# Kernel tuning notes

Measured on AMD Instinct MI355X. Metric: run time of the kernel, lower is better.

## Reference

```python
import jax, jax.numpy as jnp
import numpy as np

B, S, M = 128, 4096, 20
LOG_2PI = float(np.log(2.0 * np.pi))


def setup_inputs() -> dict:
    key = jax.random.key(0)
    k1, k2, k3, k4, k5 = jax.random.split(key, 5)
    xs = jax.random.normal(k1, (B, S, 5), dtype=jnp.float32)
    logits_pred = jax.random.normal(k2, (B, S, M), dtype=jnp.float32)
    mus_pred = jax.random.normal(k3, (B, S, M, 2), dtype=jnp.float32)
    # sigmas are Cholesky entries (l00, l10, l11); diagonal must be positive.
    sigmas_pred = jax.random.uniform(k4, (B, S, M, 3), dtype=jnp.float32) + 0.1
    pen_pred = jax.random.uniform(k5, (B, S, 3), dtype=jnp.float32)
    return {"xs": xs, "logits_pred": logits_pred, "mus_pred": mus_pred,
            "sigmas_pred": sigmas_pred, "pen_pred": pen_pred}


def reference(xs, logits_pred, mus_pred, sigmas_pred, pen_pred):
    # split stroke-5 format: (dx_abs, dy_abs) + 3 pen states
    position_true = xs[..., :2]          # [B,S,2]
    pen_true = xs[..., 2:]               # [B,S,3]

    # relative positions: roll by 1 along seq, first step prev = (0,0)
    position_prev = jnp.concatenate(
        [jnp.zeros_like(position_true[:, :1]), position_true[:, :-1]], axis=1)
    rel = position_true - position_prev  # [B,S,2]

    # closed-form 2D Gaussian log-density with lower-tri Cholesky
    # scale_tril entries (tril_indices(2,2) order): l00, l10, l11
    l00 = sigmas_pred[..., 0]            # [B,S,M]
    l10 = sigmas_pred[..., 1]
    l11 = sigmas_pred[..., 2]
    d = rel[:, :, None, :] - mus_pred    # [B,S,M,2]
    z0 = d[..., 0] / l00
    z1 = (d[..., 1] - l10 * z0) / l11
    comp_logp = (-0.5 * (z0 * z0 + z1 * z1)
                 - LOG_2PI - jnp.log(l00) - jnp.log(l11))  # [B,S,M]

    # mixture log-prob via logsumexp over components
    mix_logp = jax.nn.logsumexp(
        jax.nn.log_softmax(logits_pred, axis=-1) + comp_logp, axis=-1)  # [B,S]
    position_loss = -jnp.sum(mix_logp)

    # pen loss: faithful to source -> CrossEntropyLoss(input=pen_true, target=pen_pred)
    # (soft-target CE, mean reduction over B*S rows)
    logp = jax.nn.log_softmax(pen_true.reshape(-1, 3), axis=-1)
    pen_loss = jnp.mean(-jnp.sum(pen_pred.reshape(-1, 3) * logp, axis=-1))

    return position_loss + pen_loss
```

## Files before the change

kernel.cpp:

```cpp
#include <hip/hip_runtime.h>
#include <math.h>

#define BB 128
#define SS 4096
#define MM 20
#define NPOS (BB * SS)
#define BLOCK 256
#define NBLOCKS (NPOS / BLOCK)

__device__ __forceinline__ float fast_rcp(float x) { return __builtin_amdgcn_rcpf(x); }

__global__ __launch_bounds__(BLOCK) void sketch_main(
    const float* __restrict__ xs,
    const float* __restrict__ logits,
    const float* __restrict__ mus,
    const float* __restrict__ sigmas,
    const float* __restrict__ pen_pred,
    float* __restrict__ partials)
{
    const float LOG_2PI = 1.8378770664093453f;
    int idx = blockIdx.x * BLOCK + threadIdx.x;
    int s = idx & (SS - 1);

    const float* xp = xs + (size_t)idx * 5;
    float px  = xp[0], py  = xp[1];
    float pt0 = xp[2], pt1 = xp[3], pt2 = xp[4];
    float qx = 0.0f, qy = 0.0f;
    if (s != 0) { qx = xp[-5]; qy = xp[-4]; }
    float rx = px - qx, ry = py - qy;

    const float4* lp = (const float4*)(logits + (size_t)idx * 20);
    float lg[20];
#pragma unroll
    for (int i = 0; i < 5; ++i) {
        float4 v = lp[i];
        lg[4*i+0]=v.x; lg[4*i+1]=v.y; lg[4*i+2]=v.z; lg[4*i+3]=v.w;
    }
    const float4* mp = (const float4*)(mus + (size_t)idx * 40);
    float mu[40];
#pragma unroll
    for (int i = 0; i < 10; ++i) {
        float4 v = mp[i];
        mu[4*i+0]=v.x; mu[4*i+1]=v.y; mu[4*i+2]=v.z; mu[4*i+3]=v.w;
    }
    const float4* sp = (const float4*)(sigmas + (size_t)idx * 60);
    float sg[60];
#pragma unroll
    for (int i = 0; i < 15; ++i) {
        float4 v = sp[i];
        sg[4*i+0]=v.x; sg[4*i+1]=v.y; sg[4*i+2]=v.z; sg[4*i+3]=v.w;
    }

    float a[20];
    float mx_l = -INFINITY, mx_a = -INFINITY;
#pragma unroll
    for (int m = 0; m < MM; ++m) {
        float l00 = sg[3*m+0], l10 = sg[3*m+1], l11 = sg[3*m+2];
        float dx = rx - mu[2*m+0];
        float dy = ry - mu[2*m+1];
        float z0 = dx * fast_rcp(l00);
        float z1 = (dy - l10 * z0) * fast_rcp(l11);
        float comp = -0.5f * (z0*z0 + z1*z1) - LOG_2PI - __logf(l00 * l11);
        float av = lg[m] + comp;
        a[m] = av;
        mx_l = fmaxf(mx_l, lg[m]);
        mx_a = fmaxf(mx_a, av);
    }
    float se_l = 0.0f, se_a = 0.0f;
#pragma unroll
    for (int m = 0; m < MM; ++m) {
        se_l += __expf(lg[m] - mx_l);
        se_a += __expf(a[m]  - mx_a);
    }
    float mix_logp = (mx_a + __logf(se_a)) - (mx_l + __logf(se_l));

    float pm = fmaxf(pt0, fmaxf(pt1, pt2));
    float es = __expf(pt0 - pm) + __expf(pt1 - pm) + __expf(pt2 - pm);
    float lse3 = pm + __logf(es);
    const float* pp = pen_pred + (size_t)idx * 3;
    float pen = -(pp[0]*(pt0-lse3) + pp[1]*(pt1-lse3) + pp[2]*(pt2-lse3));

    float val = -mix_logp + pen * (1.0f / (float)NPOS);

#pragma unroll
    for (int off = 32; off > 0; off >>= 1) val += __shfl_down(val, off, 64);
    __shared__ float red[BLOCK / 64];
    int lane = threadIdx.x & 63, wid = threadIdx.x >> 6;
    if (lane == 0) red[wid] = val;
    __syncthreads();
    if (threadIdx.x == 0)
        partials[blockIdx.x] = red[0] + red[1] + red[2] + red[3];
}

__global__ __launch_bounds__(BLOCK) void sketch_reduce(
    const float* __restrict__ partials, float* __restrict__ out)
{
    float v = 0.0f;
    for (int i = threadIdx.x; i < NBLOCKS; i += BLOCK) v += partials[i];
#pragma unroll
    for (int off = 32; off > 0; off >>= 1) v += __shfl_down(v, off, 64);
    __shared__ float red[BLOCK / 64];
    int lane = threadIdx.x & 63, wid = threadIdx.x >> 6;
    if (lane == 0) red[wid] = v;
    __syncthreads();
    if (threadIdx.x == 0)
        out[0] = red[0] + red[1] + red[2] + red[3];
}

extern "C" void kernel_launch(void* const* d_in, const int* in_sizes, int n_in,
                              void* d_out, int out_size, void* d_ws, size_t ws_size,
                              hipStream_t stream) {
    const float* xs       = (const float*)d_in[0];
    const float* logits   = (const float*)d_in[1];
    const float* mus      = (const float*)d_in[2];
    const float* sigmas   = (const float*)d_in[3];
    const float* pen_pred = (const float*)d_in[4];
    float* out = (float*)d_out;
    float* partials = (float*)d_ws;

    sketch_main<<<NBLOCKS, BLOCK, 0, stream>>>(xs, logits, mus, sigmas, pen_pred, partials);
    sketch_reduce<<<1, BLOCK, 0, stream>>>(partials, out);
}
```

Measured before the change: 295.9 us.

## Map mixture components to lanes with half-wave shuffle reductions

Instead of one thread handling a whole position with 120 floats in registers, each half-wave of 32 lanes now handles one position, one lane per mixture component. Max and sum reductions run through xor shuffles, and each wave loops over 64 positions. The goal is contiguous loads across lanes, lower register pressure and better occupancy. In exchange 12 of every 32 lanes sit idle, and each position pays for shuffle reductions and redundant xs/pen loads that every lane performs.

```diff
diff --git a/kernel.cpp b/kernel.cpp
--- a/kernel.cpp
+++ b/kernel.cpp
@@ -6,7 +6,9 @@
 #define MM 20
 #define NPOS (BB * SS)
 #define BLOCK 256
-#define NBLOCKS (NPOS / BLOCK)
+#define POS_PER_BLOCK 256
+#define NBLOCKS (NPOS / POS_PER_BLOCK)
+#define ITERS (POS_PER_BLOCK / 8)
 
 __device__ __forceinline__ float fast_rcp(float x) { return __builtin_amdgcn_rcpf(x); }
 
@@ -19,74 +21,66 @@
     float* __restrict__ partials)
 {
     const float LOG_2PI = 1.8378770664093453f;
-    int idx = blockIdx.x * BLOCK + threadIdx.x;
-    int s = idx & (SS - 1);
+    const int lane = threadIdx.x & 63;
+    const int wave = threadIdx.x >> 6;
+    const int half = lane >> 5;
+    const int j    = lane & 31;
+    const int wavebase = blockIdx.x * POS_PER_BLOCK + wave * 64;
 
-    const float* xp = xs + (size_t)idx * 5;
-    float px  = xp[0], py  = xp[1];
-    float pt0 = xp[2], pt1 = xp[3], pt2 = xp[4];
-    float qx = 0.0f, qy = 0.0f;
-    if (s != 0) { qx = xp[-5]; qy = xp[-4]; }
-    float rx = px - qx, ry = py - qy;
+    float acc = 0.0f;
 
-    const float4* lp = (const float4*)(logits + (size_t)idx * 20);
-    float lg[20];
+#pragma unroll 4
+    for (int t = 0; t < ITERS; ++t) {
+        const int p = wavebase + t * 2 + half;
+        const int s = p & (SS - 1);
+
+        const float* xp = xs + (size_t)p * 5;
+        float px = xp[0], py = xp[1];
+        float qx = 0.0f, qy = 0.0f;
+        if (s != 0) { qx = xp[-5]; qy = xp[-4]; }
+        float rx = px - qx, ry = py - qy;
+
+        float lgj = -INFINITY, a = -INFINITY;
+        if (j < MM) {
+            const float* sb = sigmas + (size_t)p * 60 + j * 3;
+            float l00 = sb[0], l10 = sb[1], l11 = sb[2];
+            const float* mb = mus + (size_t)p * 40 + j * 2;
+            float m0 = mb[0], m1 = mb[1];
+            lgj = logits[(size_t)p * 20 + j];
+            float z0 = (rx - m0) * fast_rcp(l00);
+            float z1 = ((ry - m1) - l10 * z0) * fast_rcp(l11);
+            a = lgj - 0.5f * (z0 * z0 + z1 * z1) - LOG_2PI - __logf(l00 * l11);
+        }
+
+        float mx_a = a, mx_l = lgj;
 #pragma unroll
-    for (int i = 0; i < 5; ++i) {
-        float4 v = lp[i];
-        lg[4*i+0]=v.x; lg[4*i+1]=v.y; lg[4*i+2]=v.z; lg[4*i+3]=v.w;
-    }
-    const float4* mp = (const float4*)(mus + (size_t)idx * 40);
-    float mu[40];
+        for (int off = 16; off; off >>= 1) {
+            mx_a = fmaxf(mx_a, __shfl_xor(mx_a, off, 32));
+            mx_l = fmaxf(mx_l, __shfl_xor(mx_l, off, 32));
+        }
+        float ea = (j < MM) ? __expf(a - mx_a)   : 0.0f;
+        float el = (j < MM) ? __expf(lgj - mx_l) : 0.0f;
 #pragma unroll
-    for (int i = 0; i < 10; ++i) {
-        float4 v = mp[i];
-        mu[4*i+0]=v.x; mu[4*i+1]=v.y; mu[4*i+2]=v.z; mu[4*i+3]=v.w;
-    }
-    const float4* sp = (const float4*)(sigmas + (size_t)idx * 60);
-    float sg[60];
-#pragma unroll
-    for (int i = 0; i < 15; ++i) {
-        float4 v = sp[i];
-        sg[4*i+0]=v.x; sg[4*i+1]=v.y; sg[4*i+2]=v.z; sg[4*i+3]=v.w;
+        for (int off = 16; off; off >>= 1) {
+            ea += __shfl_xor(ea, off, 32);
+            el += __shfl_xor(el, off, 32);
+        }
+        float mix_logp = (mx_a + __logf(ea)) - (mx_l + __logf(el));
+
+        float pt0 = xp[2], pt1 = xp[3], pt2 = xp[4];
+        float pm = fmaxf(pt0, fmaxf(pt1, pt2));
+        float lse3 = pm + __logf(__expf(pt0 - pm) + __expf(pt1 - pm) + __expf(pt2 - pm));
+        const float* pp = pen_pred + (size_t)p * 3;
+        float pen = -(pp[0] * (pt0 - lse3) + pp[1] * (pt1 - lse3) + pp[2] * (pt2 - lse3));
+
+        float val = -mix_logp + pen * (1.0f / (float)NPOS);
+        acc += (j == 0) ? val : 0.0f;
     }
 
-    float a[20];
-    float mx_l = -INFINITY, mx_a = -INFINITY;
 #pragma unroll
-    for (int m = 0; m < MM; ++m) {
-        float l00 = sg[3*m+0], l10 = sg[3*m+1], l11 = sg[3*m+2];
-        float dx = rx - mu[2*m+0];
-        float dy = ry - mu[2*m+1];
-        float z0 = dx * fast_rcp(l00);
-        float z1 = (dy - l10 * z0) * fast_rcp(l11);
-        float comp = -0.5f * (z0*z0 + z1*z1) - LOG_2PI - __logf(l00 * l11);
-        float av = lg[m] + comp;
-        a[m] = av;
-        mx_l = fmaxf(mx_l, lg[m]);
-        mx_a = fmaxf(mx_a, av);
-    }
-    float se_l = 0.0f, se_a = 0.0f;
-#pragma unroll
-    for (int m = 0; m < MM; ++m) {
-        se_l += __expf(lg[m] - mx_l);
-        se_a += __expf(a[m]  - mx_a);
-    }
-    float mix_logp = (mx_a + __logf(se_a)) - (mx_l + __logf(se_l));
-
-    float pm = fmaxf(pt0, fmaxf(pt1, pt2));
-    float es = __expf(pt0 - pm) + __expf(pt1 - pm) + __expf(pt2 - pm);
-    float lse3 = pm + __logf(es);
-    const float* pp = pen_pred + (size_t)idx * 3;
-    float pen = -(pp[0]*(pt0-lse3) + pp[1]*(pt1-lse3) + pp[2]*(pt2-lse3));
-
-    float val = -mix_logp + pen * (1.0f / (float)NPOS);
-
-#pragma unroll
-    for (int off = 32; off > 0; off >>= 1) val += __shfl_down(val, off, 64);
+    for (int off = 32; off > 0; off >>= 1) acc += __shfl_down(acc, off, 64);
     __shared__ float red[BLOCK / 64];
-    int lane = threadIdx.x & 63, wid = threadIdx.x >> 6;
-    if (lane == 0) red[wid] = val;
+    if (lane == 0) red[wave] = acc;
     __syncthreads();
     if (threadIdx.x == 0)
         partials[blockIdx.x] = red[0] + red[1] + red[2] + red[3];
```

Result: slower. 313.4 us (+5.9%).
